# Optimization experiments

Measured on AMD Instinct MI355X. Metric: run time of the kernel, lower is better.

The kernel has to match this reference:

```python
import jax, jax.numpy as jnp
import numpy as np

NUM_HEADS = 16

def setup_inputs() -> dict:
    key = jax.random.key(0)
    ks = jax.random.split(key, 8)
    T, S, B, E = 2048, 2048, 4, 1024
    s = 0.02
    return {
        "query": jax.random.normal(ks[0], (T, B, E), jnp.float32),
        "key": jax.random.normal(ks[1], (S, B, E), jnp.float32),
        "value": jax.random.normal(ks[2], (S, B, E), jnp.float32),
        "q_proj_weight": jax.random.normal(ks[3], (E, E), jnp.float32) * s,
        "k_proj_weight": jax.random.normal(ks[4], (E, E), jnp.float32) * s,
        "v_proj_weight": jax.random.normal(ks[5], (E, E), jnp.float32) * s,
        "out_proj_weight": jax.random.normal(ks[6], (E, E), jnp.float32) * s,
        "out_proj_bias": jax.random.normal(ks[7], (E,), jnp.float32) * s,
    }

def reference(query, key, value, q_proj_weight, k_proj_weight, v_proj_weight,
              out_proj_weight, out_proj_bias):
    T, B, E = query.shape
    S = key.shape[0]
    H = NUM_HEADS
    hd = E // H
    # F.linear: x @ W.T
    q = jnp.einsum('tbe,fe->tbf', query, q_proj_weight) * (float(hd) ** -0.5)
    k = jnp.einsum('sbe,fe->sbf', key, k_proj_weight)
    v = jnp.einsum('sbe,fe->sbf', value, v_proj_weight)
    # [len, B, E] -> [B*H, len, hd]  (view then transpose, as in torch)
    q = q.reshape(T, B * H, hd).transpose(1, 0, 2)
    k = k.reshape(S, B * H, hd).transpose(1, 0, 2)
    v = v.reshape(S, B * H, hd).transpose(1, 0, 2)
    scores = jnp.einsum('nth,nsh->nts', q, k)      # [B*H, T, S]
    attn = jax.nn.softmax(scores, axis=-1)          # dropout p=0.0 -> identity
    out = jnp.einsum('nts,nsh->nth', attn, v)       # [B*H, T, hd]
    out = out.transpose(1, 0, 2).reshape(T, B, E)
    attn_output = jnp.einsum('tbe,fe->tbf', out, out_proj_weight) + out_proj_bias
    # faithful to original: view(num_heads, batch, T, S) of the [B*H,T,S] buffer
    avg_weights = attn.reshape(H, B, T, S).sum(axis=0) / H  # [B, T, S]
    return attn_output, avg_weights
```

## Files before the change

### kernel.cpp

```cpp
#include <hip/hip_runtime.h>
#include <stdint.h>

#define T_LEN 2048
#define S_LEN 2048
#define BATCH 4
#define EMB 1024
#define NH 16
#define HD 64
#define MROWS 8192

typedef __attribute__((ext_vector_type(8))) __bf16 bfx8;
typedef __attribute__((ext_vector_type(4))) float fx4;
typedef __attribute__((ext_vector_type(16))) float fx16;
typedef __attribute__((ext_vector_type(8))) unsigned short usx8;
typedef __attribute__((ext_vector_type(2))) unsigned int ux2;
typedef __attribute__((ext_vector_type(4))) unsigned int ux4;

typedef __attribute__((address_space(1))) const void GV;
typedef __attribute__((address_space(3))) void LV;
#define GLL(gp, lp) __builtin_amdgcn_global_load_lds((GV*)(gp), (LV*)(lp), 16, 0, 0)

#define QSCALE 0.18033688011112042591f
#define M0F 12.0f

static __device__ __forceinline__ unsigned short f2bf(float f) {
  unsigned int u = __float_as_uint(f);
  u += 0x7fffu + ((u >> 16) & 1u);
  return (unsigned short)(u >> 16);
}

static __device__ __forceinline__ unsigned int cvt_pk(float lo, float hi) {
  unsigned int r;
  asm("v_cvt_pk_bf16_f32 %0, %1, %2" : "=v"(r) : "v"(lo), "v"(hi));
  return r;
}

static __device__ __forceinline__ void plswap(unsigned int &a, unsigned int &b) {
  auto r = __builtin_amdgcn_permlane32_swap((int)a, (int)b, false, false);
  a = (unsigned int)r[0];
  b = (unsigned int)r[1];
}

#define PIPE_BARRIER(N)                                              \
  do {                                                               \
    asm volatile("s_waitcnt vmcnt(" #N ")" ::: "memory");            \
    __builtin_amdgcn_s_barrier();                                    \
    asm volatile("" ::: "memory");                                   \
  } while (0)

__global__ __launch_bounds__(256) void cast_all(
    const float* __restrict__ q, const float* __restrict__ k, const float* __restrict__ v,
    const float* __restrict__ wq, const float* __restrict__ wk, const float* __restrict__ wv,
    const float* __restrict__ wo,
    unsigned short* __restrict__ xq, unsigned short* __restrict__ xk, unsigned short* __restrict__ xv,
    unsigned short* __restrict__ bwq, unsigned short* __restrict__ bwk, unsigned short* __restrict__ bwv,
    unsigned short* __restrict__ bwo)
{
  const long IN8 = (long)MROWS * EMB / 8;
  const long W8  = (long)EMB * EMB / 8;
  const long total = 3 * IN8 + 4 * W8;
  for (long i = (long)blockIdx.x * 256 + threadIdx.x; i < total; i += (long)gridDim.x * 256) {
    const float* s; unsigned short* d; long off;
    if (i < 3 * IN8) {
      long wch = i / IN8; off = i - wch * IN8;
      s = (wch == 0) ? q : (wch == 1) ? k : v;
      d = (wch == 0) ? xq : (wch == 1) ? xk : xv;
    } else {
      long j = i - 3 * IN8; long wch = j / W8; off = j - wch * W8;
      s = (wch == 0) ? wq : (wch == 1) ? wk : (wch == 2) ? wv : wo;
      d = (wch == 0) ? bwq : (wch == 1) ? bwk : (wch == 2) ? bwv : bwo;
    }
    const float4* sp = (const float4*)(s + off * 8);
    float4 a = sp[0], b2 = sp[1];
    usx8 r;
    r[0] = f2bf(a.x);  r[1] = f2bf(a.y);  r[2] = f2bf(a.z);  r[3] = f2bf(a.w);
    r[4] = f2bf(b2.x); r[5] = f2bf(b2.y); r[6] = f2bf(b2.z); r[7] = f2bf(b2.w);
    *(usx8*)(d + off * 8) = r;
  }
}

template<int EPI>
__global__ __launch_bounds__(256) void gemm_bt(
    const unsigned short* __restrict__ A,
    const unsigned short* __restrict__ Bw,
    void* __restrict__ Cp,
    const float* __restrict__ bias,
    float scale)
{
  __shared__ unsigned short As[3][128 * 32];
  __shared__ unsigned short Bs[3][128 * 32];
  const int tid = threadIdx.x;
  const int lane = tid & 63;
  const int w = tid >> 6, wr = w >> 1, wc = w & 1;
  const int lr = lane & 15, lhi = lane >> 4;
  const long rowA0 = (long)blockIdx.x * 128;
  const long rowB0 = (long)blockIdx.y * 128;
  fx4 acc[4][4] = {};

  auto stage = [&](int kt, int bf) {
#pragma unroll
    for (int i = 0; i < 2; ++i) {
      int c = tid + i * 256;
      int r = c >> 2, ci = c & 3;
      int cs = ci ^ ((r >> 1) & 3);
      GLL(A + (rowA0 + r) * 1024 + kt * 32 + cs * 8, &As[bf][c * 8]);
      GLL(Bw + (rowB0 + r) * 1024 + kt * 32 + cs * 8, &Bs[bf][c * 8]);
    }
  };

  stage(0, 0);
  stage(1, 1);
  for (int kt = 0; kt < 32; ++kt) {
    const int bf = kt % 3;
    if (kt < 31) PIPE_BARRIER(4); else PIPE_BARRIER(0);
    if (kt + 2 < 32) stage(kt + 2, (kt + 2) % 3);
    bfx8 af[4], bwf[4];
#pragma unroll
    for (int m = 0; m < 4; ++m) {
      int r = wr * 64 + m * 16 + lr;
      af[m] = *(const bfx8*)&As[bf][r * 32 + ((lhi ^ ((r >> 1) & 3)) * 8)];
    }
#pragma unroll
    for (int n = 0; n < 4; ++n) {
      int r = wc * 64 + n * 16 + lr;
      bwf[n] = *(const bfx8*)&Bs[bf][r * 32 + ((lhi ^ ((r >> 1) & 3)) * 8)];
    }
    __builtin_amdgcn_s_setprio(1);
#pragma unroll
    for (int m = 0; m < 4; ++m)
#pragma unroll
      for (int n = 0; n < 4; ++n)
        acc[m][n] = __builtin_amdgcn_mfma_f32_16x16x32_bf16(af[m], bwf[n], acc[m][n], 0, 0, 0);
    __builtin_amdgcn_s_setprio(0);
  }
  if (EPI == 0) {
    unsigned short* out = (unsigned short*)Cp;
#pragma unroll
    for (int m = 0; m < 4; ++m)
#pragma unroll
      for (int n = 0; n < 4; ++n)
#pragma unroll
        for (int j = 0; j < 4; ++j) {
          long row = rowA0 + wr * 64 + m * 16 + lhi * 4 + j;
          long col = rowB0 + wc * 64 + n * 16 + lr;
          long t = row >> 2, b = row & 3;
          long h = col >> 6, d = col & 63;
          out[((b * 16 + h) * 2048 + t) * 64 + d] = f2bf(acc[m][n][j] * scale);
        }
  } else if (EPI == 1) {
    float* out = (float*)Cp;
#pragma unroll
    for (int m = 0; m < 4; ++m)
#pragma unroll
      for (int n = 0; n < 4; ++n)
#pragma unroll
        for (int j = 0; j < 4; ++j) {
          long row = rowA0 + wr * 64 + m * 16 + lhi * 4 + j;
          long col = rowB0 + wc * 64 + n * 16 + lr;
          out[row * 1024 + col] = acc[m][n][j] + bias[col];
        }
  } else {
    unsigned short* out = (unsigned short*)Cp;
#pragma unroll
    for (int m = 0; m < 4; ++m)
#pragma unroll
      for (int n = 0; n < 4; ++n)
#pragma unroll
        for (int j = 0; j < 4; ++j) {
          long row = rowA0 + wr * 64 + m * 16 + lhi * 4 + j;
          long col = rowB0 + wc * 64 + n * 16 + lr;
          long s = row >> 2, b = row & 3;
          long h = col >> 6, d = col & 63;
          out[(((b * 16 + h) * 64 + d) << 11) + s] = f2bf(acc[m][n][j]);
        }
  }
}

__global__ __launch_bounds__(512, 4) void flash_fwd(
    const unsigned short* __restrict__ qs, const unsigned short* __restrict__ ks,
    const unsigned short* __restrict__ vt, unsigned short* __restrict__ os,
    float* __restrict__ lgi)
{
  __shared__ unsigned short Kl[3][64 * 64];
  __shared__ unsigned short Vl[3][64 * 64];
  const int tid = threadIdx.x;
  const int w = tid >> 6;
  const int lane = tid & 63;
  const int l31 = lane & 31;
  const int hi = lane >> 5;
  const long bh = blockIdx.x;
  const long t0 = (long)blockIdx.y * 256;
  const unsigned short* kb0 = ks + bh * 2048 * 64;
  const unsigned short* vb0 = vt + bh * 64 * 2048;

  bfx8 qf[4];
  {
    const unsigned short* qp = qs + (bh * 2048 + t0 + w * 32 + l31) * 64;
#pragma unroll
    for (int ksl = 0; ksl < 4; ++ksl)
      qf[ksl] = *(const bfx8*)(qp + ksl * 16 + hi * 8);
  }

  bfx8 ones8;
  {
    union { ux4 u; bfx8 b; } ou;
    ou.u.x = ou.u.y = ou.u.z = ou.u.w = 0x3F803F80u;
    ones8 = ou.b;
  }

  fx16 oacc[2] = {};
  fx16 lacc = {};

  auto stage = [&](int st, int bf) {
    const unsigned short* kp = kb0 + st * 64 * 64;
    const unsigned short* vp = vb0 + st * 64;
    int r = tid >> 3, pc = tid & 7;
    int cs = pc ^ (r & 7);
    GLL(kp + r * 64 + cs * 8, &Kl[bf][tid * 8]);
    GLL(vp + (long)r * 2048 + cs * 8, &Vl[bf][tid * 8]);
  };

  stage(0, 0);
  stage(1, 1);
  for (int st = 0; st < 32; ++st) {
    const int bf = st % 3;
    if (st < 31) PIPE_BARRIER(2); else PIPE_BARRIER(0);
    if (st + 2 < 32) stage(st + 2, (st + 2) % 3);
    fx16 sc[2] = {};
    __builtin_amdgcn_s_setprio(1);
#pragma unroll
    for (int ksl = 0; ksl < 4; ++ksl)
#pragma unroll
      for (int kb = 0; kb < 2; ++kb) {
        int row = kb * 32 + l31;
        int phys = (2 * ksl + hi) ^ (row & 7);
        bfx8 af = *(const bfx8*)&Kl[bf][row * 64 + phys * 8];
        sc[kb] = __builtin_amdgcn_mfma_f32_32x32x16_bf16(af, qf[ksl], sc[kb], 0, 0, 0);
      }
    __builtin_amdgcn_s_setprio(0);
#pragma unroll
    for (int kb = 0; kb < 2; ++kb)
#pragma unroll
      for (int r = 0; r < 16; ++r)
        sc[kb][r] = __builtin_amdgcn_exp2f(sc[kb][r] - M0F);
#pragma unroll
    for (int ksl = 0; ksl < 4; ++ksl) {
      const int kb = ksl >> 1;
      const int tb = 2 * (ksl & 1);
      unsigned int A0 = cvt_pk(sc[kb][tb * 4 + 0], sc[kb][tb * 4 + 1]);
      unsigned int A1 = cvt_pk(sc[kb][tb * 4 + 2], sc[kb][tb * 4 + 3]);
      unsigned int B0 = cvt_pk(sc[kb][tb * 4 + 4], sc[kb][tb * 4 + 5]);
      unsigned int B1 = cvt_pk(sc[kb][tb * 4 + 6], sc[kb][tb * 4 + 7]);
      plswap(A0, B0);
      plswap(A1, B1);
      ux4 uw; uw.x = A0; uw.y = A1; uw.z = B0; uw.w = B1;
      union { ux4 u; bfx8 b; } cvv; cvv.u = uw;
      bfx8 pa = cvv.b;
      __builtin_amdgcn_s_setprio(1);
#pragma unroll
      for (int db = 0; db < 2; ++db) {
        int row = db * 32 + l31;
        int phys = (2 * ksl + hi) ^ (row & 7);
        bfx8 vf = *(const bfx8*)&Vl[bf][row * 64 + phys * 8];
        oacc[db] = __builtin_amdgcn_mfma_f32_32x32x16_bf16(vf, pa, oacc[db], 0, 0, 0);
      }
      lacc = __builtin_amdgcn_mfma_f32_32x32x16_bf16(ones8, pa, lacc, 0, 0, 0);
      __builtin_amdgcn_s_setprio(0);
    }
  }
  const long b_ = bh >> 4, h_ = bh & 15;
  {
    float li = 1.f / lacc[0];
    long t = t0 + w * 32 + l31;
    unsigned short* ob = os + (t * 4 + b_) * 1024 + h_ * 64;
#pragma unroll
    for (int db = 0; db < 2; ++db)
#pragma unroll
      for (int tt = 0; tt < 4; ++tt) {
        int d0i = db * 32 + tt * 8 + hi * 4;
        unsigned int u0 = cvt_pk(oacc[db][tt * 4 + 0] * li, oacc[db][tt * 4 + 1] * li);
        unsigned int u1 = cvt_pk(oacc[db][tt * 4 + 2] * li, oacc[db][tt * 4 + 3] * li);
        ux2 uu; uu.x = u0; uu.y = u1;
        *(ux2*)(ob + d0i) = uu;
      }
    if (hi == 0) lgi[bh * 2048 + t] = li;
  }
}

__global__ __launch_bounds__(256, 2) void avg_kernel(
    const unsigned short* __restrict__ qs, const unsigned short* __restrict__ ks,
    const float* __restrict__ lgi, float* __restrict__ avg)
{
  __shared__ unsigned short Qs[2][128 * 64];
  __shared__ unsigned short Ks[2][128 * 64];
  __shared__ float lgl[16 * 128];
  const int tid = threadIdx.x, lane = tid & 63, w = tid >> 6;
  const int l31 = lane & 31, hi = lane >> 5;
  const long b = blockIdx.z;
  const long t0 = (long)blockIdx.x * 128;
  const long s0 = (long)blockIdx.y * 128;
  fx16 aacc[4] = {};

  auto stage = [&](int h, int bf) {
    long bh = b * 16 + h;
    const unsigned short* qb = qs + (bh * 2048 + t0) * 64;
    const unsigned short* kb = ks + (bh * 2048 + s0) * 64;
#pragma unroll
    for (int i = 0; i < 4; ++i) {
      int c = tid + i * 256, r = c >> 3, cs = (c & 7) ^ (r & 7);
      GLL(qb + r * 64 + cs * 8, &Qs[bf][c * 8]);
      GLL(kb + r * 64 + cs * 8, &Ks[bf][c * 8]);
    }
  };

#pragma unroll
  for (int i = 0; i < 2; ++i) {
    int c = tid + i * 256;
    GLL(&lgi[(b * 16 + (c >> 5)) * 2048 + t0 + (c & 31) * 4], &lgl[c * 4]);
  }
  stage(0, 0);
  __syncthreads();
  int buf = 0;
  for (int h = 0; h < 16; ++h) {
    if (h < 15) stage(h + 1, buf ^ 1);
    fx16 sacc[4] = {};
    const int arow = w * 32 + l31;
    __builtin_amdgcn_s_setprio(1);
#pragma unroll
    for (int ksl = 0; ksl < 4; ++ksl) {
      bfx8 aq = *(const bfx8*)&Qs[buf][arow * 64 + (((2 * ksl + hi) ^ (arow & 7)) * 8)];
#pragma unroll
      for (int n = 0; n < 4; ++n) {
        int brow = n * 32 + l31;
        bfx8 bk = *(const bfx8*)&Ks[buf][brow * 64 + (((2 * ksl + hi) ^ (brow & 7)) * 8)];
        sacc[n] = __builtin_amdgcn_mfma_f32_32x32x16_bf16(aq, bk, sacc[n], 0, 0, 0);
      }
    }
    __builtin_amdgcn_s_setprio(0);
#pragma unroll
    for (int r = 0; r < 16; ++r) {
      float lj = lgl[h * 128 + w * 32 + (r & 3) + 8 * (r >> 2) + 4 * hi];
#pragma unroll
      for (int n = 0; n < 4; ++n)
        aacc[n][r] += __builtin_amdgcn_exp2f(sacc[n][r] - M0F) * lj;
    }
    __syncthreads();
    buf ^= 1;
  }
#pragma unroll
  for (int r = 0; r < 16; ++r) {
    long t = t0 + w * 32 + (r & 3) + 8 * (r >> 2) + 4 * hi;
#pragma unroll
    for (int n = 0; n < 4; ++n)
      avg[(b * 2048 + t) * 2048 + s0 + n * 32 + l31] = aacc[n][r] * 0.0625f;
  }
}

extern "C" void kernel_launch(void* const* d_in, const int* in_sizes, int n_in,
                              void* d_out, int out_size, void* d_ws, size_t ws_size,
                              hipStream_t stream)
{
  const float* q   = (const float*)d_in[0];
  const float* k   = (const float*)d_in[1];
  const float* v   = (const float*)d_in[2];
  const float* wq  = (const float*)d_in[3];
  const float* wk  = (const float*)d_in[4];
  const float* wv  = (const float*)d_in[5];
  const float* wo  = (const float*)d_in[6];
  const float* bias= (const float*)d_in[7];
  char* ws = (char*)d_ws;
  const long MB = 1024 * 1024;
  unsigned short* bwq = (unsigned short*)(ws + 0 * MB);
  unsigned short* bwk = (unsigned short*)(ws + 2 * MB);
  unsigned short* bwv = (unsigned short*)(ws + 4 * MB);
  unsigned short* bwo = (unsigned short*)(ws + 6 * MB);
  unsigned short* xq  = (unsigned short*)(ws + 8 * MB);
  unsigned short* xk  = (unsigned short*)(ws + 24 * MB);
  unsigned short* xv  = (unsigned short*)(ws + 40 * MB);
  unsigned short* qsb = (unsigned short*)(ws + 56 * MB);
  unsigned short* ksb = (unsigned short*)(ws + 72 * MB);
  unsigned short* vtb = (unsigned short*)(ws + 104 * MB);
  unsigned short* osb = (unsigned short*)(ws + 120 * MB);
  float* lgi = (float*)(ws + 137 * MB);
  float* outp = (float*)d_out;

  cast_all<<<14336, 256, 0, stream>>>(q, k, v, wq, wk, wv, wo,
                                      xq, xk, xv, bwq, bwk, bwv, bwo);
  dim3 gg(64, 8);
  gemm_bt<0><<<gg, 256, 0, stream>>>(xq, bwq, qsb, nullptr, QSCALE);
  gemm_bt<0><<<gg, 256, 0, stream>>>(xk, bwk, ksb, nullptr, 1.0f);
  gemm_bt<2><<<gg, 256, 0, stream>>>(xv, bwv, vtb, nullptr, 1.0f);
  flash_fwd<<<dim3(64, 8), 512, 0, stream>>>(qsb, ksb, vtb, osb, lgi);
  avg_kernel<<<dim3(16, 16, 4), 256, 0, stream>>>(qsb, ksb, lgi, outp + 8388608);
  gemm_bt<1><<<gg, 256, 0, stream>>>(osb, bwo, d_out, bias, 1.0f);
}
```

Measured before the change: 300.8 us.

## Fuse fp32-to-bf16 activation cast into a single batched QKV projection GEMM

Removes the standalone cast pass over query/key/value. The QKV GEMM now loads fp32 activations directly, converts them to bf16 in registers and writes them into swizzled LDS. The three projection GEMMs are merged into one launch indexed by blockIdx.z, and weights get their own small cast kernel. This trades the intermediate bf16 write and reread for register-staged A loads, double instead of triple buffering, and reading fp32 A twice as wide.

```diff
diff --git a/kernel.cpp b/kernel.cpp
--- a/kernel.cpp
+++ b/kernel.cpp
@@ -48,44 +48,151 @@
     asm volatile("" ::: "memory");                                   \
   } while (0)
 
-__global__ __launch_bounds__(256) void cast_all(
-    const float* __restrict__ q, const float* __restrict__ k, const float* __restrict__ v,
-    const float* __restrict__ wq, const float* __restrict__ wk, const float* __restrict__ wv,
-    const float* __restrict__ wo,
-    unsigned short* __restrict__ xq, unsigned short* __restrict__ xk, unsigned short* __restrict__ xv,
-    unsigned short* __restrict__ bwq, unsigned short* __restrict__ bwk, unsigned short* __restrict__ bwv,
-    unsigned short* __restrict__ bwo)
-{
-  const long IN8 = (long)MROWS * EMB / 8;
-  const long W8  = (long)EMB * EMB / 8;
-  const long total = 3 * IN8 + 4 * W8;
-  for (long i = (long)blockIdx.x * 256 + threadIdx.x; i < total; i += (long)gridDim.x * 256) {
-    const float* s; unsigned short* d; long off;
-    if (i < 3 * IN8) {
-      long wch = i / IN8; off = i - wch * IN8;
-      s = (wch == 0) ? q : (wch == 1) ? k : v;
-      d = (wch == 0) ? xq : (wch == 1) ? xk : xv;
-    } else {
-      long j = i - 3 * IN8; long wch = j / W8; off = j - wch * W8;
-      s = (wch == 0) ? wq : (wch == 1) ? wk : (wch == 2) ? wv : wo;
-      d = (wch == 0) ? bwq : (wch == 1) ? bwk : (wch == 2) ? bwv : bwo;
-    }
-    const float4* sp = (const float4*)(s + off * 8);
-    float4 a = sp[0], b2 = sp[1];
-    usx8 r;
-    r[0] = f2bf(a.x);  r[1] = f2bf(a.y);  r[2] = f2bf(a.z);  r[3] = f2bf(a.w);
-    r[4] = f2bf(b2.x); r[5] = f2bf(b2.y); r[6] = f2bf(b2.z); r[7] = f2bf(b2.w);
-    *(usx8*)(d + off * 8) = r;
-  }
-}
-
-template<int EPI>
-__global__ __launch_bounds__(256) void gemm_bt(
+__global__ __launch_bounds__(256) void cast_w(
+    const float* __restrict__ wq, const float* __restrict__ wk,
+    const float* __restrict__ wv, const float* __restrict__ wo,
+    unsigned short* __restrict__ bwq, unsigned short* __restrict__ bwk,
+    unsigned short* __restrict__ bwv, unsigned short* __restrict__ bwo)
+{
+  const long W8 = (long)EMB * EMB / 8;
+  long i = (long)blockIdx.x * 256 + threadIdx.x;
+  long wch = i / W8, off = i - wch * W8;
+  const float* s = (wch == 0) ? wq : (wch == 1) ? wk : (wch == 2) ? wv : wo;
+  unsigned short* d = (wch == 0) ? bwq : (wch == 1) ? bwk : (wch == 2) ? bwv : bwo;
+  const float4* sp = (const float4*)(s + off * 8);
+  float4 a = sp[0], b2 = sp[1];
+  usx8 r;
+  r[0] = f2bf(a.x);  r[1] = f2bf(a.y);  r[2] = f2bf(a.z);  r[3] = f2bf(a.w);
+  r[4] = f2bf(b2.x); r[5] = f2bf(b2.y); r[6] = f2bf(b2.z); r[7] = f2bf(b2.w);
+  *(usx8*)(d + off * 8) = r;
+}
+
+__global__ __launch_bounds__(256) void qkv_gemm(
+    const float* __restrict__ qA, const float* __restrict__ kA, const float* __restrict__ vA,
+    const unsigned short* __restrict__ bwq, const unsigned short* __restrict__ bwk,
+    const unsigned short* __restrict__ bwv,
+    unsigned short* __restrict__ qsb, unsigned short* __restrict__ ksb,
+    unsigned short* __restrict__ vtb)
+{
+  __shared__ unsigned short As[2][128 * 32];
+  __shared__ unsigned short Bs[2][128 * 32];
+  const int tid = threadIdx.x;
+  const int z = blockIdx.z;
+  const float* A = (z == 0) ? qA : (z == 1) ? kA : vA;
+  const unsigned short* Bw = (z == 0) ? bwq : (z == 1) ? bwk : bwv;
+  const int lane = tid & 63;
+  const int w = tid >> 6, wr = w >> 1, wc = w & 1;
+  const int lr = lane & 15, lhi = lane >> 4;
+  const long rowA0 = (long)blockIdx.x * 128;
+  const long rowB0 = (long)blockIdx.y * 128;
+  fx4 acc[4][4] = {};
+
+  float4 ra[2][2];
+  auto loadA = [&](int kt) {
+#pragma unroll
+    for (int i = 0; i < 2; ++i) {
+      int c = tid + i * 256;
+      int r = c >> 2, ci = c & 3;
+      const float4* p = (const float4*)(A + (rowA0 + r) * 1024 + kt * 32 + ci * 8);
+      ra[i][0] = p[0];
+      ra[i][1] = p[1];
+    }
+  };
+  auto writeA = [&](int bf) {
+#pragma unroll
+    for (int i = 0; i < 2; ++i) {
+      int c = tid + i * 256;
+      int r = c >> 2, ci = c & 3;
+      int phys = ci ^ ((r >> 1) & 3);
+      ux4 u;
+      u.x = cvt_pk(ra[i][0].x, ra[i][0].y);
+      u.y = cvt_pk(ra[i][0].z, ra[i][0].w);
+      u.z = cvt_pk(ra[i][1].x, ra[i][1].y);
+      u.w = cvt_pk(ra[i][1].z, ra[i][1].w);
+      *(ux4*)&As[bf][(r * 4 + phys) * 8] = u;
+    }
+  };
+  auto stageB = [&](int kt, int bf) {
+#pragma unroll
+    for (int i = 0; i < 2; ++i) {
+      int c = tid + i * 256;
+      int r = c >> 2, ci = c & 3;
+      int cs = ci ^ ((r >> 1) & 3);
+      GLL(Bw + (rowB0 + r) * 1024 + kt * 32 + cs * 8, &Bs[bf][c * 8]);
+    }
+  };
+
+  loadA(0);
+  stageB(0, 0);
+  writeA(0);
+  asm volatile("s_waitcnt vmcnt(0) lgkmcnt(0)" ::: "memory");
+  __builtin_amdgcn_s_barrier();
+  asm volatile("" ::: "memory");
+
+  for (int kt = 0; kt < 32; ++kt) {
+    const int bf = kt & 1;
+    if (kt < 31) { loadA(kt + 1); stageB(kt + 1, bf ^ 1); }
+    bfx8 af[4], bwf[4];
+#pragma unroll
+    for (int m = 0; m < 4; ++m) {
+      int r = wr * 64 + m * 16 + lr;
+      af[m] = *(const bfx8*)&As[bf][r * 32 + ((lhi ^ ((r >> 1) & 3)) * 8)];
+    }
+#pragma unroll
+    for (int n = 0; n < 4; ++n) {
+      int r = wc * 64 + n * 16 + lr;
+      bwf[n] = *(const bfx8*)&Bs[bf][r * 32 + ((lhi ^ ((r >> 1) & 3)) * 8)];
+    }
+    __builtin_amdgcn_s_setprio(1);
+#pragma unroll
+    for (int m = 0; m < 4; ++m)
+#pragma unroll
+      for (int n = 0; n < 4; ++n)
+        acc[m][n] = __builtin_amdgcn_mfma_f32_16x16x32_bf16(af[m], bwf[n], acc[m][n], 0, 0, 0);
+    __builtin_amdgcn_s_setprio(0);
+    if (kt < 31) {
+      writeA(bf ^ 1);
+      asm volatile("s_waitcnt vmcnt(0) lgkmcnt(0)" ::: "memory");
+      __builtin_amdgcn_s_barrier();
+      asm volatile("" ::: "memory");
+    }
+  }
+  const float scale = (z == 0) ? QSCALE : 1.0f;
+  if (z < 2) {
+    unsigned short* out = (z == 0) ? qsb : ksb;
+#pragma unroll
+    for (int m = 0; m < 4; ++m)
+#pragma unroll
+      for (int n = 0; n < 4; ++n)
+#pragma unroll
+        for (int j = 0; j < 4; ++j) {
+          long row = rowA0 + wr * 64 + m * 16 + lhi * 4 + j;
+          long col = rowB0 + wc * 64 + n * 16 + lr;
+          long t = row >> 2, b = row & 3;
+          long h = col >> 6, d = col & 63;
+          out[((b * 16 + h) * 2048 + t) * 64 + d] = f2bf(acc[m][n][j] * scale);
+        }
+  } else {
+#pragma unroll
+    for (int m = 0; m < 4; ++m)
+#pragma unroll
+      for (int n = 0; n < 4; ++n)
+#pragma unroll
+        for (int j = 0; j < 4; ++j) {
+          long row = rowA0 + wr * 64 + m * 16 + lhi * 4 + j;
+          long col = rowB0 + wc * 64 + n * 16 + lr;
+          long s = row >> 2, b = row & 3;
+          long h = col >> 6, d = col & 63;
+          vtb[(((b * 16 + h) * 64 + d) << 11) + s] = f2bf(acc[m][n][j]);
+        }
+  }
+}
+
+__global__ __launch_bounds__(256) void gemm_out(
     const unsigned short* __restrict__ A,
     const unsigned short* __restrict__ Bw,
-    void* __restrict__ Cp,
-    const float* __restrict__ bias,
-    float scale)
+    float* __restrict__ out,
+    const float* __restrict__ bias)
 {
   __shared__ unsigned short As[3][128 * 32];
   __shared__ unsigned short Bs[3][128 * 32];
@@ -133,47 +240,16 @@
         acc[m][n] = __builtin_amdgcn_mfma_f32_16x16x32_bf16(af[m], bwf[n], acc[m][n], 0, 0, 0);
     __builtin_amdgcn_s_setprio(0);
   }
-  if (EPI == 0) {
-    unsigned short* out = (unsigned short*)Cp;
-#pragma unroll
-    for (int m = 0; m < 4; ++m)
-#pragma unroll
-      for (int n = 0; n < 4; ++n)
-#pragma unroll
-        for (int j = 0; j < 4; ++j) {
-          long row = rowA0 + wr * 64 + m * 16 + lhi * 4 + j;
-          long col = rowB0 + wc * 64 + n * 16 + lr;
-          long t = row >> 2, b = row & 3;
-          long h = col >> 6, d = col & 63;
-          out[((b * 16 + h) * 2048 + t) * 64 + d] = f2bf(acc[m][n][j] * scale);
-        }
-  } else if (EPI == 1) {
-    float* out = (float*)Cp;
-#pragma unroll
-    for (int m = 0; m < 4; ++m)
-#pragma unroll
-      for (int n = 0; n < 4; ++n)
-#pragma unroll
-        for (int j = 0; j < 4; ++j) {
-          long row = rowA0 + wr * 64 + m * 16 + lhi * 4 + j;
-          long col = rowB0 + wc * 64 + n * 16 + lr;
-          out[row * 1024 + col] = acc[m][n][j] + bias[col];
-        }
-  } else {
-    unsigned short* out = (unsigned short*)Cp;
-#pragma unroll
-    for (int m = 0; m < 4; ++m)
-#pragma unroll
-      for (int n = 0; n < 4; ++n)
-#pragma unroll
-        for (int j = 0; j < 4; ++j) {
-          long row = rowA0 + wr * 64 + m * 16 + lhi * 4 + j;
-          long col = rowB0 + wc * 64 + n * 16 + lr;
-          long s = row >> 2, b = row & 3;
-          long h = col >> 6, d = col & 63;
-          out[(((b * 16 + h) * 64 + d) << 11) + s] = f2bf(acc[m][n][j]);
-        }
-  }
+#pragma unroll
+  for (int m = 0; m < 4; ++m)
+#pragma unroll
+    for (int n = 0; n < 4; ++n)
+#pragma unroll
+      for (int j = 0; j < 4; ++j) {
+        long row = rowA0 + wr * 64 + m * 16 + lhi * 4 + j;
+        long col = rowB0 + wc * 64 + n * 16 + lr;
+        out[row * 1024 + col] = acc[m][n][j] + bias[col];
+      }
 }
 
 __global__ __launch_bounds__(512, 4) void flash_fwd(
@@ -374,9 +450,6 @@
   unsigned short* bwk = (unsigned short*)(ws + 2 * MB);
   unsigned short* bwv = (unsigned short*)(ws + 4 * MB);
   unsigned short* bwo = (unsigned short*)(ws + 6 * MB);
-  unsigned short* xq  = (unsigned short*)(ws + 8 * MB);
-  unsigned short* xk  = (unsigned short*)(ws + 24 * MB);
-  unsigned short* xv  = (unsigned short*)(ws + 40 * MB);
   unsigned short* qsb = (unsigned short*)(ws + 56 * MB);
   unsigned short* ksb = (unsigned short*)(ws + 72 * MB);
   unsigned short* vtb = (unsigned short*)(ws + 104 * MB);
@@ -384,13 +457,9 @@
   float* lgi = (float*)(ws + 137 * MB);
   float* outp = (float*)d_out;
 
-  cast_all<<<14336, 256, 0, stream>>>(q, k, v, wq, wk, wv, wo,
-                                      xq, xk, xv, bwq, bwk, bwv, bwo);
-  dim3 gg(64, 8);
-  gemm_bt<0><<<gg, 256, 0, stream>>>(xq, bwq, qsb, nullptr, QSCALE);
-  gemm_bt<0><<<gg, 256, 0, stream>>>(xk, bwk, ksb, nullptr, 1.0f);
-  gemm_bt<2><<<gg, 256, 0, stream>>>(xv, bwv, vtb, nullptr, 1.0f);
+  cast_w<<<2048, 256, 0, stream>>>(wq, wk, wv, wo, bwq, bwk, bwv, bwo);
+  qkv_gemm<<<dim3(64, 8, 3), 256, 0, stream>>>(q, k, v, bwq, bwk, bwv, qsb, ksb, vtb);
   flash_fwd<<<dim3(64, 8), 512, 0, stream>>>(qsb, ksb, vtb, osb, lgi);
   avg_kernel<<<dim3(16, 16, 4), 256, 0, stream>>>(qsb, ksb, lgi, outp + 8388608);
-  gemm_bt<1><<<gg, 256, 0, stream>>>(osb, bwo, d_out, bias, 1.0f);
-}
+  gemm_out<<<dim3(64, 8), 256, 0, stream>>>(osb, bwo, (float*)d_out, bias);
+}
```

After: 282.1 us. -6.2%, faster.
